# Kernel optimization log

Hardware: AMD Instinct MI355X
Metric: run time of the kernel (lower is better)

Reference implementation:

```python
import jax, jax.numpy as jnp
import numpy as np

N, D, H, L = 50000, 128, 4, 3
E = 800000
C = D // H            # head dim = 32
NEG_SLOPE = 0.2       # PyG GATv2Conv default negative_slope
LN_EPS = 1e-5         # nn.LayerNorm default eps


def setup_inputs() -> dict:
    key = jax.random.key(0)
    ks = jax.random.split(key, 8)
    s = 1.0 / np.sqrt(D).astype(np.float32)
    return {
        "fine_poi_x": jax.random.normal(ks[0], (N, D), jnp.float32),
        "edge_index": jax.random.randint(ks[1], (2, E), 0, N, dtype=jnp.int32),
        "Wl": jax.random.normal(ks[2], (L, D, D), jnp.float32) * s,
        "bl": jnp.zeros((L, D), jnp.float32),
        "Wr": jax.random.normal(ks[3], (L, D, D), jnp.float32) * s,
        "br": jnp.zeros((L, D), jnp.float32),
        "att": jax.random.normal(ks[4], (L, H, C), jnp.float32) * s,
        "bias": jnp.zeros((L, D), jnp.float32),
        "gamma": jnp.ones((L, D), jnp.float32),
        "beta": jnp.zeros((L, D), jnp.float32),
    }


def _gatv2_conv(x, src, dst, Wl, bl, Wr, br, att, bias):
    # x: [N, D]; src/dst: [E'] (self-loops already appended)
    xl = (x @ Wl + bl).reshape(N, H, C)   # source-side transform (lin_l)
    xr = (x @ Wr + br).reshape(N, H, C)   # target-side transform (lin_r)
    m = xl[src] + xr[dst]                 # [E', H, C] per-edge pre-activation
    m = jax.nn.leaky_relu(m, NEG_SLOPE)
    e = jnp.einsum("ehc,hc->eh", m, att)  # [E', H] attention logits
    # segment softmax over edges grouped by destination node
    emax = jax.ops.segment_max(e, dst, num_segments=N)      # [N, H]
    ee = jnp.exp(e - emax[dst])
    denom = jax.ops.segment_sum(ee, dst, num_segments=N)    # [N, H]
    alpha = ee / denom[dst]               # self-loops guarantee denom >= 1 term
    out = jax.ops.segment_sum(xl[src] * alpha[:, :, None], dst, num_segments=N)
    return out.reshape(N, D) + bias


def _layernorm(x, g, b):
    mu = jnp.mean(x, axis=-1, keepdims=True)
    var = jnp.var(x, axis=-1, keepdims=True)
    return (x - mu) * jax.lax.rsqrt(var + LN_EPS) * g + b


def reference(fine_poi_x, edge_index, Wl, bl, Wr, br, att, bias, gamma, beta):
    # PyG GATv2Conv add_self_loops=True: append i->i edges
    loops = jnp.arange(N, dtype=edge_index.dtype)
    src = jnp.concatenate([edge_index[0], loops])
    dst = jnp.concatenate([edge_index[1], loops])
    x = fine_poi_x
    for i in range(L):
        h = _gatv2_conv(x, src, dst, Wl[i], bl[i], Wr[i], br[i], att[i], bias[i])
        x = _layernorm(x + h, gamma[i], beta[i])
        if i != L - 1:
            x = jax.nn.relu(x)
    return x
```

## Files before the change

kernel.cpp:

```cpp
#include <hip/hip_runtime.h>

#define N_NODES 50000
#define N_EDGES 800000
#define DIM 128
#define TOT_EDGES (N_EDGES + N_NODES)
#define LOG2E 1.44269504088896f

#define BSHIFT 9
#define BNODES 512
#define NB ((N_NODES + BNODES - 1) / BNODES)
#define BCAP 16384
#define EPB 4096
#define EPT 16
#define NBLK_A ((TOT_EDGES + EPB - 1) / EPB)
#define CONVX_BLOCKS ((N_NODES * (DIM / 2) + 255) / 256)
#define CONVW_BLOCKS ((3 * 2 * DIM * DIM + 255) / 256)

typedef __attribute__((ext_vector_type(8))) _Float16 f16x8;
typedef __attribute__((ext_vector_type(2))) _Float16 h2;
typedef __attribute__((ext_vector_type(4))) float f32x4;
typedef decltype(__builtin_amdgcn_cvt_pkrtz(0.f, 0.f)) fp16v2;

__device__ inline uint h2u(h2 v) { return __builtin_bit_cast(uint, v); }
__device__ inline h2 u2h(uint v) { return __builtin_bit_cast(h2, v); }
__device__ inline uint pk2u(fp16v2 v) { return __builtin_bit_cast(uint, v); }

__device__ inline float rowsum16(float v) {
  int x;
  x = __builtin_amdgcn_update_dpp(0, __float_as_int(v), 0x128, 0xF, 0xF, true);
  v += __int_as_float(x);
  x = __builtin_amdgcn_update_dpp(0, __float_as_int(v), 0x124, 0xF, 0xF, true);
  v += __int_as_float(x);
  x = __builtin_amdgcn_update_dpp(0, __float_as_int(v), 0x122, 0xF, 0xF, true);
  v += __int_as_float(x);
  x = __builtin_amdgcn_update_dpp(0, __float_as_int(v), 0x121, 0xF, 0xF, true);
  v += __int_as_float(x);
  return v;
}

__device__ inline float quadsum4(float v) {
  int x;
  x = __builtin_amdgcn_update_dpp(0, __float_as_int(v), 0xB1, 0xF, 0xF, true);
  v += __int_as_float(x);
  x = __builtin_amdgcn_update_dpp(0, __float_as_int(v), 0x4E, 0xF, 0xF, true);
  v += __int_as_float(x);
  return v;
}


__global__ __launch_bounds__(256) void conv_kernel(const float* __restrict__ x,
                                                   uint* __restrict__ xb,
                                                   int* __restrict__ bcnt,
                                                   const float* __restrict__ Wl,
                                                   const float* __restrict__ Wr,
                                                   ushort* __restrict__ Wt,
                                                   const float* __restrict__ att,
                                                   uint* __restrict__ attc,
                                                   uint* __restrict__ col) {
  int b = blockIdx.x;
  if (b < CONVX_BLOCKS) {
    if (b == 0 && threadIdx.x < NB) bcnt[threadIdx.x] = 0;
    int t = b * 256 + threadIdx.x;
    if (t < N_NODES * (DIM / 2)) {
      float2 v = ((const float2*)x)[t];
      xb[t] = pk2u(__builtin_amdgcn_cvt_pkrtz(v.x, v.y));
    }
  } else {
    int bb = b - CONVX_BLOCKS;
    if (bb == 0) {
      int u = threadIdx.x;
      if (u < 192) {
        float a0 = att[2 * u] * LOG2E, a1 = att[2 * u + 1] * LOG2E;
        attc[u] = pk2u(__builtin_amdgcn_cvt_pkrtz(a0, a1));
      }
      if (u < 64) col[TOT_EDGES + u] = 0u;
    }
    int t = bb * 256 + threadIdx.x;
    if (t < 3 * 2 * DIM * DIM) {
      int k = t & 127;
      int n = (t >> 7) & 127;
      int w = (t >> 14) & 1;
      int l = t >> 15;
      const float* W = w ? Wr : Wl;
      _Float16 h = (_Float16)W[l * DIM * DIM + k * DIM + n];
      Wt[t] = __builtin_bit_cast(ushort, h);
    }
  }
}


__global__ __launch_bounds__(256) void partA_kernel(const int* __restrict__ srcArr,
                                                    const int* __restrict__ dstArr,
                                                    int* __restrict__ bcnt,
                                                    uint* __restrict__ bbuf) {
  int tid = threadIdx.x;
  int e0 = blockIdx.x * EPB;
  __shared__ int hist[NB], base[NB], loff[NB];
  if (tid < NB) { hist[tid] = 0; loff[tid] = 0; }
  __syncthreads();

  int sv[EPT], dv[EPT];
#pragma unroll
  for (int i = 0; i < EPT; ++i) {
    int e = e0 + i * 256 + tid;
    int s = 0, d = -1;
    if (e < TOT_EDGES) {
      if (e < N_EDGES) { s = srcArr[e]; d = dstArr[e]; }
      else { s = e - N_EDGES; d = s; }
    }
    sv[i] = s; dv[i] = d;
    if (d >= 0) atomicAdd(&hist[d >> BSHIFT], 1);
  }
  __syncthreads();
  if (tid < NB) {
    int h = hist[tid];
    if (h > 0) base[tid] = atomicAdd(&bcnt[tid], h);
  }
  __syncthreads();
#pragma unroll
  for (int i = 0; i < EPT; ++i) {
    int d = dv[i];
    if (d >= 0) {
      int b = d >> BSHIFT;
      int p = atomicAdd(&loff[b], 1);
      bbuf[(size_t)b * BCAP + base[b] + p] = ((uint)sv[i] << 9) | (uint)(d & (BNODES - 1));
    }
  }
}


__global__ __launch_bounds__(512) void partB_kernel(const uint* __restrict__ bbuf,
                                                    const int* __restrict__ bcnt,
                                                    int* __restrict__ rowptr,
                                                    uint* __restrict__ col) {
  int b = blockIdx.x, tid = threadIdx.x;

  __shared__ int s[128];
  if (tid < 128) s[tid] = (tid < NB) ? bcnt[tid] : 0;
  __syncthreads();
  for (int off = 1; off < 128; off <<= 1) {
    int t = 0;
    if (tid < 128 && tid >= off) t = s[tid - off];
    __syncthreads();
    if (tid < 128) s[tid] += t;
    __syncthreads();
  }
  int cb = (b > 0) ? s[b - 1] : 0;
  int m = bcnt[b];
  if (b == 0 && tid == 0) rowptr[N_NODES] = TOT_EDGES;
  const uint* buf = bbuf + (size_t)b * BCAP;

  __shared__ int cnt[BNODES], scn[BNODES], cur[BNODES];
  cnt[tid] = 0;
  __syncthreads();
  for (int e = tid; e < m; e += 512) {
    atomicAdd(&cnt[buf[e] & (BNODES - 1)], 1);
  }
  __syncthreads();
  int c = cnt[tid];
  scn[tid] = c;
  __syncthreads();
  for (int off = 1; off < BNODES; off <<= 1) {
    int t = (tid >= off) ? scn[tid - off] : 0;
    __syncthreads();
    scn[tid] += t;
    __syncthreads();
  }
  int excl = scn[tid] - c;
  int node = b * BNODES + tid;
  if (node < N_NODES) rowptr[node] = cb + excl;
  cur[tid] = excl;
  __syncthreads();
  for (int e = tid; e < m; e += 512) {
    uint sd = buf[e];
    int p = atomicAdd(&cur[sd & (BNODES - 1)], 1);
    col[cb + p] = (sd >> 9) << 4;
  }
}


__global__ __launch_bounds__(256) void gemm_mfma_kernel(
    const uint* __restrict__ xb,
    const ushort* __restrict__ Wt,
    const float* __restrict__ bl, const float* __restrict__ br,
    uint* __restrict__ xl, uint* __restrict__ xr) {
  int wave = threadIdx.x >> 6, lane = threadIdx.x & 63;
  int lr = lane & 15, kq = lane >> 4;
  int m0 = blockIdx.x * 64;

  const ushort* W = Wt + (wave >> 1) * (DIM * DIM);
  const float* bias = (wave >> 1) ? br : bl;
  uint* outp = (wave >> 1) ? xr : xl;
  int n0 = (wave & 1) * 64;
  const ushort* xbp = (const ushort*)xb;

  f16x8 bfrag[4][4];
#pragma unroll
  for (int nt = 0; nt < 4; ++nt)
#pragma unroll
    for (int kt = 0; kt < 4; ++kt)
      bfrag[nt][kt] = *(const f16x8*)(W + (n0 + nt * 16 + lr) * DIM + kt * 32 + kq * 8);

  f32x4 acc[4][4];
#pragma unroll
  for (int mt = 0; mt < 4; ++mt)
#pragma unroll
    for (int nt = 0; nt < 4; ++nt)
      acc[mt][nt] = (f32x4){0.f, 0.f, 0.f, 0.f};

  f16x8 af[4];
  {
    int m = m0 + lr;
    int mc = m < N_NODES ? m : N_NODES - 1;
#pragma unroll
    for (int kt = 0; kt < 4; ++kt)
      af[kt] = *(const f16x8*)(xbp + (size_t)mc * DIM + kt * 32 + kq * 8);
  }
#pragma unroll
  for (int mt = 0; mt < 4; ++mt) {
    f16x8 afn[4];
    if (mt < 3) {
      int m2 = m0 + (mt + 1) * 16 + lr;
      int mc2 = m2 < N_NODES ? m2 : N_NODES - 1;
#pragma unroll
      for (int kt = 0; kt < 4; ++kt)
        afn[kt] = *(const f16x8*)(xbp + (size_t)mc2 * DIM + kt * 32 + kq * 8);
    }
#pragma unroll
    for (int nt = 0; nt < 4; ++nt)
#pragma unroll
      for (int kt = 0; kt < 4; ++kt)
        acc[mt][nt] = __builtin_amdgcn_mfma_f32_16x16x32_f16(bfrag[nt][kt], af[kt],
                                                             acc[mt][nt], 0, 0, 0);
    if (mt < 3) {
      af[0] = afn[0]; af[1] = afn[1]; af[2] = afn[2]; af[3] = afn[3];
    }
  }

#pragma unroll
  for (int mt = 0; mt < 4; ++mt) {
    int m = m0 + mt * 16 + lr;
    if (m < N_NODES) {
#pragma unroll
      for (int nt = 0; nt < 4; ++nt) {
        int n = n0 + nt * 16 + kq * 4;
        float4 bb = *(const float4*)(bias + n);
        uint2 o;
        o.x = pk2u(__builtin_amdgcn_cvt_pkrtz(acc[mt][nt][0] + bb.x, acc[mt][nt][1] + bb.y));
        o.y = pk2u(__builtin_amdgcn_cvt_pkrtz(acc[mt][nt][2] + bb.z, acc[mt][nt][3] + bb.w));
        *(uint2*)(outp + (size_t)m * (DIM / 2) + (n >> 1)) = o;
      }
    }
  }
}


__global__ __launch_bounds__(64) void att_kernel(
    const uint4* __restrict__ xinb, const uint4* __restrict__ xlb,
    const uint4* __restrict__ xrb, const int* __restrict__ rowptr,
    const uint* __restrict__ col, const uint4* __restrict__ attc,
    const float4* __restrict__ bias, const float4* __restrict__ gamma,
    const float4* __restrict__ beta, uint4* __restrict__ xoutb,
    float4* __restrict__ xoutf, int do_relu) {
  int lane = threadIdx.x;
  uint j = (uint)(lane & 15);
  int e4 = lane >> 4;
  int n = blockIdx.x;

  uint4 rq = xrb[(uint)(n * 16) + j];
  uint4 aq = attc[j];
  h2 r2[4] = {u2h(rq.x), u2h(rq.y), u2h(rq.z), u2h(rq.w)};
  h2 at2[4] = {u2h(aq.x), u2h(aq.y), u2h(aq.z), u2h(aq.w)};
  const h2 c02 = {(_Float16)0.2f, (_Float16)0.2f};

  h2 accp[4] = {};
  float den = 0.f;

  int js = rowptr[n], je = rowptr[n + 1];

  uint c0 = col[(uint)(js + e4)];
  uint c1 = col[(uint)(js + 4 + e4)];
  uint c2 = col[(uint)(js + 8 + e4)];
  uint c3 = col[(uint)(js + 12 + e4)];
  uint c4 = col[(uint)(js + 16 + e4)];
  uint c5 = col[(uint)(js + 20 + e4)];
  uint c6 = col[(uint)(js + 24 + e4)];
  uint4 g0 = xlb[c0 + j];
  uint4 g1 = xlb[c1 + j];
  uint4 g2 = xlb[c2 + j];
  uint4 g3 = xlb[c3 + j];
  uint4 g4 = xlb[c4 + j];

  for (int cbase = js; cbase < je; cbase += 4) {
    uint cn = col[(uint)(cbase + 28 + e4)];
    uint4 gn = xlb[c5 + j];

    h2 a0 = u2h(g0.x), a1 = u2h(g0.y), a2 = u2h(g0.z), a3 = u2h(g0.w);
    float p = 0.f;
    {
      h2 s0 = a0 + r2[0], s1 = a1 + r2[1], s2 = a2 + r2[2], s3 = a3 + r2[3];
      h2 m0 = __builtin_elementwise_max(s0, s0 * c02);
      h2 m1 = __builtin_elementwise_max(s1, s1 * c02);
      h2 m2 = __builtin_elementwise_max(s2, s2 * c02);
      h2 m3 = __builtin_elementwise_max(s3, s3 * c02);
      p = __builtin_amdgcn_fdot2(__builtin_bit_cast(fp16v2, m0),
                                 __builtin_bit_cast(fp16v2, at2[0]), p, false);
      p = __builtin_amdgcn_fdot2(__builtin_bit_cast(fp16v2, m1),
                                 __builtin_bit_cast(fp16v2, at2[1]), p, false);
      p = __builtin_amdgcn_fdot2(__builtin_bit_cast(fp16v2, m2),
                                 __builtin_bit_cast(fp16v2, at2[2]), p, false);
      p = __builtin_amdgcn_fdot2(__builtin_bit_cast(fp16v2, m3),
                                 __builtin_bit_cast(fp16v2, at2[3]), p, false);
    }
    p = quadsum4(p);
    float w = (cbase + e4 < je) ? __builtin_amdgcn_exp2f(p) : 0.f;
    den += w;
    _Float16 wh = (_Float16)w;
    h2 w2 = {wh, wh};
    accp[0] = w2 * a0 + accp[0];
    accp[1] = w2 * a1 + accp[1];
    accp[2] = w2 * a2 + accp[2];
    accp[3] = w2 * a3 + accp[3];

    g0 = g1; g1 = g2; g2 = g3; g3 = g4; g4 = gn;
    c5 = c6; c6 = cn;
  }

#pragma unroll
  for (int t = 0; t < 4; ++t) {
    accp[t] += u2h((uint)__shfl_xor((int)h2u(accp[t]), 16, 64));
    accp[t] += u2h((uint)__shfl_xor((int)h2u(accp[t]), 32, 64));
  }
  den += __shfl_xor(den, 16, 64);
  den += __shfl_xor(den, 32, 64);

  float inv = 1.0f / den;
  float acc[8];
#pragma unroll
  for (int t = 0; t < 4; ++t) {
    acc[2 * t] = (float)accp[t].x;
    acc[2 * t + 1] = (float)accp[t].y;
  }

  uint4 xi4 = xinb[(uint)(n * 16) + j];
  h2 xi[4] = {u2h(xi4.x), u2h(xi4.y), u2h(xi4.z), u2h(xi4.w)};
  float4 b0 = bias[2 * j], b1 = bias[2 * j + 1];

  float o[8];
  o[0] = fmaf(acc[0], inv, b0.x + (float)xi[0].x);
  o[1] = fmaf(acc[1], inv, b0.y + (float)xi[0].y);
  o[2] = fmaf(acc[2], inv, b0.z + (float)xi[1].x);
  o[3] = fmaf(acc[3], inv, b0.w + (float)xi[1].y);
  o[4] = fmaf(acc[4], inv, b1.x + (float)xi[2].x);
  o[5] = fmaf(acc[5], inv, b1.y + (float)xi[2].y);
  o[6] = fmaf(acc[6], inv, b1.z + (float)xi[3].x);
  o[7] = fmaf(acc[7], inv, b1.w + (float)xi[3].y);

  float s1 = 0.f, s2 = 0.f;
#pragma unroll
  for (int t = 0; t < 8; ++t) { s1 += o[t]; s2 = fmaf(o[t], o[t], s2); }
  s1 = rowsum16(s1);
  s2 = rowsum16(s2);
  float mean = s1 * (1.0f / DIM);
  float var = s2 * (1.0f / DIM) - mean * mean;
  float rstd = rsqrtf(var + 1e-5f);

  float4 g0_ = gamma[2 * j], g1_ = gamma[2 * j + 1];
  float4 t0 = beta[2 * j], t1 = beta[2 * j + 1];
  float y[8];
  y[0] = (o[0] - mean) * rstd * g0_.x + t0.x;
  y[1] = (o[1] - mean) * rstd * g0_.y + t0.y;
  y[2] = (o[2] - mean) * rstd * g0_.z + t0.z;
  y[3] = (o[3] - mean) * rstd * g0_.w + t0.w;
  y[4] = (o[4] - mean) * rstd * g1_.x + t1.x;
  y[5] = (o[5] - mean) * rstd * g1_.y + t1.y;
  y[6] = (o[6] - mean) * rstd * g1_.z + t1.z;
  y[7] = (o[7] - mean) * rstd * g1_.w + t1.w;
  if (do_relu) {
#pragma unroll
    for (int t = 0; t < 8; ++t) y[t] = fmaxf(y[t], 0.f);
  }

  if (e4 == 0) {
    if (xoutb) {
      uint4 ov;
      ov.x = pk2u(__builtin_amdgcn_cvt_pkrtz(y[0], y[1]));
      ov.y = pk2u(__builtin_amdgcn_cvt_pkrtz(y[2], y[3]));
      ov.z = pk2u(__builtin_amdgcn_cvt_pkrtz(y[4], y[5]));
      ov.w = pk2u(__builtin_amdgcn_cvt_pkrtz(y[6], y[7]));
      xoutb[(uint)(n * 16) + j] = ov;
    }
    if (xoutf) {
      xoutf[(uint)(n * 32) + 2 * j] = make_float4(y[0], y[1], y[2], y[3]);
      xoutf[(uint)(n * 32) + 2 * j + 1] = make_float4(y[4], y[5], y[6], y[7]);
    }
  }
}


extern "C" void kernel_launch(void* const* d_in, const int* in_sizes, int n_in,
                              void* d_out, int out_size, void* d_ws, size_t ws_size,
                              hipStream_t stream) {
  const float* x_in  = (const float*)d_in[0];
  const int*   eidx  = (const int*)d_in[1];
  const float* Wl    = (const float*)d_in[2];
  const float* bl    = (const float*)d_in[3];
  const float* Wr    = (const float*)d_in[4];
  const float* br    = (const float*)d_in[5];
  const float* att   = (const float*)d_in[6];
  const float* bias  = (const float*)d_in[7];
  const float* gamma = (const float*)d_in[8];
  const float* beta  = (const float*)d_in[9];
  float* out = (float*)d_out;

  char* p = (char*)d_ws;
  auto alloc = [&](size_t bytes) {
    char* q = p;
    p += (bytes + 255) & ~(size_t)255;
    return q;
  };
  uint*  xb       = (uint*)alloc((size_t)N_NODES * (DIM / 2) * 4);
  uint*  xlb      = (uint*)alloc((size_t)N_NODES * (DIM / 2) * 4);
  uint*  xrb      = (uint*)alloc((size_t)N_NODES * (DIM / 2) * 4);
  ushort* Wt      = (ushort*)alloc((size_t)3 * 2 * DIM * DIM * 2);
  uint*  attc     = (uint*)alloc((size_t)3 * 64 * 4);
  int*   rowptr   = (int*)alloc((size_t)(N_NODES + 1) * 4);
  uint*  col      = (uint*)alloc((size_t)(TOT_EDGES + 64) * 4);
  uint*  bbuf     = (uint*)alloc((size_t)NB * BCAP * 4);
  int*   bcnt     = (int*)alloc((size_t)NB * 4);

  conv_kernel<<<CONVX_BLOCKS + CONVW_BLOCKS, 256, 0, stream>>>(
      x_in, xb, bcnt, Wl, Wr, Wt, att, attc, col);
  partA_kernel<<<NBLK_A, 256, 0, stream>>>(eidx, eidx + N_EDGES, bcnt, bbuf);
  partB_kernel<<<NB, 512, 0, stream>>>(bbuf, bcnt, rowptr, col);

  for (int l = 0; l < 3; ++l) {
    gemm_mfma_kernel<<<(N_NODES + 63) / 64, 256, 0, stream>>>(
        xb, Wt + (size_t)l * 2 * DIM * DIM, bl + l * DIM, br + l * DIM, xlb, xrb);
    att_kernel<<<N_NODES, 64, 0, stream>>>(
        (const uint4*)xb, (const uint4*)xlb, (const uint4*)xrb, rowptr, col,
        (const uint4*)(attc + l * 64), (const float4*)(bias + l * DIM),
        (const float4*)(gamma + l * DIM), (const float4*)(beta + l * DIM),
        (l == 2) ? nullptr : (uint4*)xb, (l == 2) ? (float4*)out : nullptr,
        (l != 2) ? 1 : 0);
  }
}
```

Measured before the change: 238.9 us.

## Split attention per head with head-major xl layout and separate LayerNorm epilogue

Stores xl in a head-major layout (each head's 32 features contiguous per node) and launches one 64-thread block per (head, node), with 16 edges processed in parallel per iteration. The aim is to shrink the gather footprint per node-head and raise the number of edges in flight, improving locality of the random gathers. The normalized aggregation goes to a staging buffer, and a new epilogue kernel applies bias, residual, LayerNorm and ReLU. This adds an extra kernel launch per layer and a round trip through the staging buffer, four times as many attention blocks, and a shallower prefetch pipeline than the previous five-deep one.

```diff
diff --git a/kernel.cpp b/kernel.cpp
--- a/kernel.cpp
+++ b/kernel.cpp
@@ -174,7 +174,7 @@
   for (int e = tid; e < m; e += 512) {
     uint sd = buf[e];
     int p = atomicAdd(&cur[sd & (BNODES - 1)], 1);
-    col[cb + p] = (sd >> 9) << 4;
+    col[cb + p] = (sd >> 9) << 2;
   }
 }
 
@@ -183,14 +183,15 @@
     const uint* __restrict__ xb,
     const ushort* __restrict__ Wt,
     const float* __restrict__ bl, const float* __restrict__ br,
-    uint* __restrict__ xl, uint* __restrict__ xr) {
+    uint* __restrict__ xlh,
+    uint* __restrict__ xr) {
   int wave = threadIdx.x >> 6, lane = threadIdx.x & 63;
   int lr = lane & 15, kq = lane >> 4;
   int m0 = blockIdx.x * 64;
 
+  bool isR = (wave >> 1) != 0;
   const ushort* W = Wt + (wave >> 1) * (DIM * DIM);
-  const float* bias = (wave >> 1) ? br : bl;
-  uint* outp = (wave >> 1) ? xr : xl;
+  const float* bias = isR ? br : bl;
   int n0 = (wave & 1) * 64;
   const ushort* xbp = (const ushort*)xb;
 
@@ -248,54 +249,54 @@
         uint2 o;
         o.x = pk2u(__builtin_amdgcn_cvt_pkrtz(acc[mt][nt][0] + bb.x, acc[mt][nt][1] + bb.y));
         o.y = pk2u(__builtin_amdgcn_cvt_pkrtz(acc[mt][nt][2] + bb.z, acc[mt][nt][3] + bb.w));
-        *(uint2*)(outp + (size_t)m * (DIM / 2) + (n >> 1)) = o;
+        if (!isR) {
+          int head = n >> 5;
+          uint base = (uint)head * (N_NODES * 16) + (uint)m * 16 + ((uint)(n & 31) >> 1);
+          *(uint2*)(xlh + base) = o;
+        } else {
+          *(uint2*)(xr + (size_t)m * (DIM / 2) + (n >> 1)) = o;
+        }
       }
     }
   }
 }
 
 
-__global__ __launch_bounds__(64) void att_kernel(
-    const uint4* __restrict__ xinb, const uint4* __restrict__ xlb,
-    const uint4* __restrict__ xrb, const int* __restrict__ rowptr,
-    const uint* __restrict__ col, const uint4* __restrict__ attc,
-    const float4* __restrict__ bias, const float4* __restrict__ gamma,
-    const float4* __restrict__ beta, uint4* __restrict__ xoutb,
-    float4* __restrict__ xoutf, int do_relu) {
+__global__ __launch_bounds__(64) void atth_kernel(
+    const uint4* __restrict__ xlh,
+    const uint4* __restrict__ xrb,
+    const int* __restrict__ rowptr, const uint* __restrict__ col,
+    const uint4* __restrict__ attc,
+    uint4* __restrict__ hstage) {
   int lane = threadIdx.x;
-  uint j = (uint)(lane & 15);
-  int e4 = lane >> 4;
-  int n = blockIdx.x;
-
-  uint4 rq = xrb[(uint)(n * 16) + j];
-  uint4 aq = attc[j];
+  int j4 = lane & 3, e16 = lane >> 2;
+  int bid = blockIdx.x;
+  int h = bid / N_NODES;
+  int n = bid - h * N_NODES;
+
+  uint4 rq = xrb[(uint)n * 16 + h * 4 + j4];
+  uint4 aq = attc[h * 4 + j4];
   h2 r2[4] = {u2h(rq.x), u2h(rq.y), u2h(rq.z), u2h(rq.w)};
   h2 at2[4] = {u2h(aq.x), u2h(aq.y), u2h(aq.z), u2h(aq.w)};
   const h2 c02 = {(_Float16)0.2f, (_Float16)0.2f};
+  const uint4* xh = xlh + (size_t)h * (N_NODES * 4);
 
   h2 accp[4] = {};
   float den = 0.f;
 
   int js = rowptr[n], je = rowptr[n + 1];
 
-  uint c0 = col[(uint)(js + e4)];
-  uint c1 = col[(uint)(js + 4 + e4)];
-  uint c2 = col[(uint)(js + 8 + e4)];
-  uint c3 = col[(uint)(js + 12 + e4)];
-  uint c4 = col[(uint)(js + 16 + e4)];
-  uint c5 = col[(uint)(js + 20 + e4)];
-  uint c6 = col[(uint)(js + 24 + e4)];
-  uint4 g0 = xlb[c0 + j];
-  uint4 g1 = xlb[c1 + j];
-  uint4 g2 = xlb[c2 + j];
-  uint4 g3 = xlb[c3 + j];
-  uint4 g4 = xlb[c4 + j];
-
-  for (int cbase = js; cbase < je; cbase += 4) {
-    uint cn = col[(uint)(cbase + 28 + e4)];
-    uint4 gn = xlb[c5 + j];
-
-    h2 a0 = u2h(g0.x), a1 = u2h(g0.y), a2 = u2h(g0.z), a3 = u2h(g0.w);
+  uint cA = col[(uint)(js + e16)];
+  bool vA = (js + e16) < je;
+  uint4 gA = xh[(vA ? cA : 0u) + (uint)j4];
+
+  for (int cbase = js; cbase < je; cbase += 16) {
+    int nb = cbase + 16;
+    uint cB = col[(uint)(nb + e16)];
+    bool vB = (nb + e16) < je;
+    uint4 gB = xh[(vB ? cB : 0u) + (uint)j4];
+
+    h2 a0 = u2h(gA.x), a1 = u2h(gA.y), a2 = u2h(gA.z), a3 = u2h(gA.w);
     float p = 0.f;
     {
       h2 s0 = a0 + r2[0], s1 = a1 + r2[1], s2 = a2 + r2[2], s3 = a3 + r2[3];
@@ -313,7 +314,7 @@
                                  __builtin_bit_cast(fp16v2, at2[3]), p, false);
     }
     p = quadsum4(p);
-    float w = (cbase + e4 < je) ? __builtin_amdgcn_exp2f(p) : 0.f;
+    float w = vA ? __builtin_amdgcn_exp2f(p) : 0.f;
     den += w;
     _Float16 wh = (_Float16)w;
     h2 w2 = {wh, wh};
@@ -322,79 +323,66 @@
     accp[2] = w2 * a2 + accp[2];
     accp[3] = w2 * a3 + accp[3];
 
-    g0 = g1; g1 = g2; g2 = g3; g3 = g4; g4 = gn;
-    c5 = c6; c6 = cn;
+    gA = gB; vA = vB;
   }
 
 #pragma unroll
   for (int t = 0; t < 4; ++t) {
+    accp[t] += u2h((uint)__shfl_xor((int)h2u(accp[t]), 4, 64));
+    accp[t] += u2h((uint)__shfl_xor((int)h2u(accp[t]), 8, 64));
     accp[t] += u2h((uint)__shfl_xor((int)h2u(accp[t]), 16, 64));
     accp[t] += u2h((uint)__shfl_xor((int)h2u(accp[t]), 32, 64));
   }
+  den += __shfl_xor(den, 4, 64);
+  den += __shfl_xor(den, 8, 64);
   den += __shfl_xor(den, 16, 64);
   den += __shfl_xor(den, 32, 64);
 
-  float inv = 1.0f / den;
-  float acc[8];
-#pragma unroll
-  for (int t = 0; t < 4; ++t) {
-    acc[2 * t] = (float)accp[t].x;
-    acc[2 * t + 1] = (float)accp[t].y;
-  }
-
-  uint4 xi4 = xinb[(uint)(n * 16) + j];
-  h2 xi[4] = {u2h(xi4.x), u2h(xi4.y), u2h(xi4.z), u2h(xi4.w)};
-  float4 b0 = bias[2 * j], b1 = bias[2 * j + 1];
-
-  float o[8];
-  o[0] = fmaf(acc[0], inv, b0.x + (float)xi[0].x);
-  o[1] = fmaf(acc[1], inv, b0.y + (float)xi[0].y);
-  o[2] = fmaf(acc[2], inv, b0.z + (float)xi[1].x);
-  o[3] = fmaf(acc[3], inv, b0.w + (float)xi[1].y);
-  o[4] = fmaf(acc[4], inv, b1.x + (float)xi[2].x);
-  o[5] = fmaf(acc[5], inv, b1.y + (float)xi[2].y);
-  o[6] = fmaf(acc[6], inv, b1.z + (float)xi[3].x);
-  o[7] = fmaf(acc[7], inv, b1.w + (float)xi[3].y);
-
-  float s1 = 0.f, s2 = 0.f;
-#pragma unroll
-  for (int t = 0; t < 8; ++t) { s1 += o[t]; s2 = fmaf(o[t], o[t], s2); }
+  if (e16 == 0) {
+    float inv = 1.0f / den;
+    uint4 ov;
+    ov.x = pk2u(__builtin_amdgcn_cvt_pkrtz((float)accp[0].x * inv, (float)accp[0].y * inv));
+    ov.y = pk2u(__builtin_amdgcn_cvt_pkrtz((float)accp[1].x * inv, (float)accp[1].y * inv));
+    ov.z = pk2u(__builtin_amdgcn_cvt_pkrtz((float)accp[2].x * inv, (float)accp[2].y * inv));
+    ov.w = pk2u(__builtin_amdgcn_cvt_pkrtz((float)accp[3].x * inv, (float)accp[3].y * inv));
+    hstage[(uint)n * 16 + h * 4 + j4] = ov;
+  }
+}
+
+
+__global__ __launch_bounds__(256) void epi_kernel(
+    const uint* __restrict__ hstage, const uint* __restrict__ xinb,
+    const float2* __restrict__ bias, const float2* __restrict__ gamma,
+    const float2* __restrict__ beta, uint* __restrict__ xoutb,
+    float2* __restrict__ xoutf, int do_relu) {
+  int lane = threadIdx.x & 63;
+  int n = blockIdx.x * 4 + (threadIdx.x >> 6);
+  size_t rowp = (size_t)n * 64 + lane;
+
+  h2 hv = u2h(hstage[rowp]);
+  h2 xi = u2h(xinb[rowp]);
+  float2 bi = bias[lane];
+  float o0 = (float)hv.x + bi.x + (float)xi.x;
+  float o1 = (float)hv.y + bi.y + (float)xi.y;
+
+  float s1 = o0 + o1, s2 = o0 * o0 + o1 * o1;
   s1 = rowsum16(s1);
   s2 = rowsum16(s2);
+  s1 += __shfl_xor(s1, 16, 64);
+  s2 += __shfl_xor(s2, 16, 64);
+  s1 += __shfl_xor(s1, 32, 64);
+  s2 += __shfl_xor(s2, 32, 64);
   float mean = s1 * (1.0f / DIM);
   float var = s2 * (1.0f / DIM) - mean * mean;
   float rstd = rsqrtf(var + 1e-5f);
 
-  float4 g0_ = gamma[2 * j], g1_ = gamma[2 * j + 1];
-  float4 t0 = beta[2 * j], t1 = beta[2 * j + 1];
-  float y[8];
-  y[0] = (o[0] - mean) * rstd * g0_.x + t0.x;
-  y[1] = (o[1] - mean) * rstd * g0_.y + t0.y;
-  y[2] = (o[2] - mean) * rstd * g0_.z + t0.z;
-  y[3] = (o[3] - mean) * rstd * g0_.w + t0.w;
-  y[4] = (o[4] - mean) * rstd * g1_.x + t1.x;
-  y[5] = (o[5] - mean) * rstd * g1_.y + t1.y;
-  y[6] = (o[6] - mean) * rstd * g1_.z + t1.z;
-  y[7] = (o[7] - mean) * rstd * g1_.w + t1.w;
-  if (do_relu) {
-#pragma unroll
-    for (int t = 0; t < 8; ++t) y[t] = fmaxf(y[t], 0.f);
-  }
-
-  if (e4 == 0) {
-    if (xoutb) {
-      uint4 ov;
-      ov.x = pk2u(__builtin_amdgcn_cvt_pkrtz(y[0], y[1]));
-      ov.y = pk2u(__builtin_amdgcn_cvt_pkrtz(y[2], y[3]));
-      ov.z = pk2u(__builtin_amdgcn_cvt_pkrtz(y[4], y[5]));
-      ov.w = pk2u(__builtin_amdgcn_cvt_pkrtz(y[6], y[7]));
-      xoutb[(uint)(n * 16) + j] = ov;
-    }
-    if (xoutf) {
-      xoutf[(uint)(n * 32) + 2 * j] = make_float4(y[0], y[1], y[2], y[3]);
-      xoutf[(uint)(n * 32) + 2 * j + 1] = make_float4(y[4], y[5], y[6], y[7]);
-    }
-  }
+  float2 gm = gamma[lane];
+  float2 bt = beta[lane];
+  float y0 = (o0 - mean) * rstd * gm.x + bt.x;
+  float y1 = (o1 - mean) * rstd * gm.y + bt.y;
+  if (do_relu) { y0 = fmaxf(y0, 0.f); y1 = fmaxf(y1, 0.f); }
+  if (xoutb) xoutb[rowp] = pk2u(__builtin_amdgcn_cvt_pkrtz(y0, y1));
+  if (xoutf) xoutf[rowp] = make_float2(y0, y1);
 }
 
 
@@ -419,9 +407,10 @@
     p += (bytes + 255) & ~(size_t)255;
     return q;
   };
-  uint*  xb       = (uint*)alloc((size_t)N_NODES * (DIM / 2) * 4);
-  uint*  xlb      = (uint*)alloc((size_t)N_NODES * (DIM / 2) * 4);
-  uint*  xrb      = (uint*)alloc((size_t)N_NODES * (DIM / 2) * 4);
+  uint*  xb       = (uint*)alloc((size_t)N_NODES * 64 * 4);
+  uint*  xlh      = (uint*)alloc((size_t)4 * N_NODES * 16 * 4);
+  uint*  xrb      = (uint*)alloc((size_t)N_NODES * 64 * 4);
+  uint*  hstage   = (uint*)alloc((size_t)N_NODES * 64 * 4);
   ushort* Wt      = (ushort*)alloc((size_t)3 * 2 * DIM * DIM * 2);
   uint*  attc     = (uint*)alloc((size_t)3 * 64 * 4);
   int*   rowptr   = (int*)alloc((size_t)(N_NODES + 1) * 4);
@@ -436,12 +425,14 @@
 
   for (int l = 0; l < 3; ++l) {
     gemm_mfma_kernel<<<(N_NODES + 63) / 64, 256, 0, stream>>>(
-        xb, Wt + (size_t)l * 2 * DIM * DIM, bl + l * DIM, br + l * DIM, xlb, xrb);
-    att_kernel<<<N_NODES, 64, 0, stream>>>(
-        (const uint4*)xb, (const uint4*)xlb, (const uint4*)xrb, rowptr, col,
-        (const uint4*)(attc + l * 64), (const float4*)(bias + l * DIM),
-        (const float4*)(gamma + l * DIM), (const float4*)(beta + l * DIM),
-        (l == 2) ? nullptr : (uint4*)xb, (l == 2) ? (float4*)out : nullptr,
+        xb, Wt + (size_t)l * 2 * DIM * DIM, bl + l * DIM, br + l * DIM, xlh, xrb);
+    atth_kernel<<<4 * N_NODES, 64, 0, stream>>>(
+        (const uint4*)xlh, (const uint4*)xrb, rowptr, col,
+        (const uint4*)(attc + l * 64), (uint4*)hstage);
+    epi_kernel<<<(N_NODES + 3) / 4, 256, 0, stream>>>(
+        hstage, xb, (const float2*)(bias + l * DIM),
+        (const float2*)(gamma + l * DIM), (const float2*)(beta + l * DIM),
+        (l == 2) ? nullptr : xb, (l == 2) ? (float2*)out : nullptr,
         (l != 2) ? 1 : 0);
   }
 }
```

Result: slower. 312.5 us (+30.8%).
